# Performance work log

Hardware: AMD Instinct MI355X
Metric: run time of the kernel (lower is better)

Reference implementation:

```python
import jax, jax.numpy as jnp
import numpy as np

V, E, H, L, P, N = 500000, 128, 128, 10, 10, 50
SCALE = 1e-4


def setup_inputs() -> dict:
    key = jax.random.key(0)
    ks = jax.random.split(key, 10)
    initrange = 0.5 / E
    return {
        "phr_inds": jax.random.randint(ks[0], (L,), 0, V),
        "pos_inds": jax.random.randint(ks[1], (P, L), 0, V),
        "neg_inds": jax.random.randint(ks[2], (N, L), 0, V),
        "u_emb": jax.random.uniform(ks[3], (V, E), minval=-initrange, maxval=initrange, dtype=jnp.float32),
        "v_emb": jax.random.uniform(ks[4], (V, E), minval=-initrange, maxval=initrange, dtype=jnp.float32),
        "w_ih": jax.random.uniform(ks[5], (3 * H, E), minval=-SCALE, maxval=SCALE, dtype=jnp.float32),
        "w_hh": jax.random.uniform(ks[6], (3 * H, H), minval=-SCALE, maxval=SCALE, dtype=jnp.float32),
        "b_ih": jax.random.uniform(ks[7], (3 * H,), minval=-SCALE, maxval=SCALE, dtype=jnp.float32),
        "b_hh": jax.random.uniform(ks[8], (3 * H,), minval=-SCALE, maxval=SCALE, dtype=jnp.float32),
        "h0": jax.random.uniform(ks[9], (H,), minval=-SCALE, maxval=SCALE, dtype=jnp.float32),
    }


def _gru_last_hidden(x, h0, w_ih, w_hh, b_ih, b_hh):
    # x: [B, L, E] -> last hidden state [B, H]; torch GRU gate order (r, z, n)
    B = x.shape[0]
    gi = jnp.einsum('ble,ge->blg', x, w_ih) + b_ih  # input projections precomputed [B, L, 3H]
    h = jnp.broadcast_to(h0, (B, h0.shape[-1]))

    def step(h, gi_t):
        gh = h @ w_hh.T + b_hh
        ir, iz, in_ = jnp.split(gi_t, 3, axis=-1)
        hr, hz, hn = jnp.split(gh, 3, axis=-1)
        r = jax.nn.sigmoid(ir + hr)
        z = jax.nn.sigmoid(iz + hz)
        n = jnp.tanh(in_ + r * hn)
        return (1.0 - z) * n + z * h, None

    h, _ = jax.lax.scan(step, h, jnp.swapaxes(gi, 0, 1))  # scan over time
    return h


def reference(phr_inds, pos_inds, neg_inds, u_emb, v_emb, w_ih, w_hh, b_ih, b_hh, h0):
    rnn_size = h0.shape[-1]
    phr_x = u_emb[phr_inds][None]   # [1, L, E] (center phrase uses u table)
    pos_x = v_emb[pos_inds]         # [P, L, E]
    neg_x = v_emb[neg_inds]         # [N, L, E]
    x = jnp.concatenate([phr_x, pos_x, neg_x], axis=0)  # batch all GRU calls together
    enc = _gru_last_hidden(x, h0, w_ih, w_hh, b_ih, b_hh)
    node = enc[0]
    n_pos = pos_inds.shape[0]
    pos_e, neg_e = enc[1:1 + n_pos], enc[1 + n_pos:]
    # dot_product_sum(exp=False): sum_i <node, pos_i> / rnn_size
    pos_loss = ((node * pos_e).sum(-1) / rnn_size).sum()
    # dot_product_sum(exp=True): exp(s) masked to s>0, then summed
    s = (node * neg_e).sum(-1) / rnn_size
    neg_sum = (jnp.exp(s) * (s > 0.0).astype(s.dtype)).sum()
    neg_loss = -jnp.log(1.0 + neg_sum)
    return -(neg_loss + pos_loss)
```

## Files before the change

kernel.cpp:

```cpp
#include <hip/hip_runtime.h>
#include <hip/hip_bf16.h>
#include <math.h>

#define V_SZ 500000
#define E_SZ 128
#define H_SZ 128
#define L_SZ 10
#define P_SZ 10
#define N_SZ 50
#define NSEQ (P_SZ + N_SZ)
#define NBLK 60
#define TPB  384

#define SIG_STRIDE 8
#define FLAG_MAGIC 0x9E370000u

#define GI_STR 388
#define XS_STR 136

typedef __attribute__((ext_vector_type(8))) short bf16x8;
typedef __attribute__((ext_vector_type(4))) float f32x4;

#define MFMA(a, b, c) __builtin_amdgcn_mfma_f32_16x16x32_bf16((a), (b), (c), 0, 0, 0)

__device__ __forceinline__ float sigmoidf(float x) {
    return 1.0f / (1.0f + expf(-x));
}

__device__ __forceinline__ unsigned short f2bf(float f) {
    __hip_bfloat16 h = __float2bfloat16(f);
    unsigned short u;
    __builtin_memcpy(&u, &h, sizeof(u));
    return u;
}

__device__ __forceinline__ unsigned f2bf2(float lo, float hi) {
    float2 v = make_float2(lo, hi);
    __hip_bfloat162 h2 = __float22bfloat162_rn(v);
    unsigned u;
    __builtin_memcpy(&u, &h2, sizeof(u));
    return u;
}

__device__ __forceinline__ uint2 f2bf4(float4 v) {
    uint2 r;
    r.x = f2bf2(v.x, v.y);
    r.y = f2bf2(v.z, v.w);
    return r;
}

__global__ __launch_bounds__(TPB) void gru_fused(
    const int*   __restrict__ phr_inds,
    const int*   __restrict__ pos_inds,
    const int*   __restrict__ neg_inds,
    const float* __restrict__ u_emb,
    const float* __restrict__ v_emb,
    const float* __restrict__ w_ih,
    const float* __restrict__ w_hh,
    const float* __restrict__ b_ih,
    const float* __restrict__ b_hh,
    const float* __restrict__ h0,
    unsigned long long* __restrict__ sig,
    float*       __restrict__ out)
{
    __shared__ __align__(16) unsigned short stage_u[384 * E_SZ];
    __shared__ __align__(16) unsigned short xs_bf16[2][16 * XS_STR];
    __shared__ __align__(16) float          gh_s[2][3 * H_SZ];
    __shared__ __align__(16) unsigned short hs_bf16[2][H_SZ];
    __shared__ __align__(16) float          node[2][H_SZ];

    float* gi_all = (float*)stage_u;

    const int bj   = blockIdx.x;
    const int seqB = bj + 1;
    const int t    = threadIdx.x;
    const int lane = t & 63;
    const int wv   = t >> 6;
    const int kg   = lane >> 4;
    const int col  = lane & 15;
    const int arow = wv * 64 + col;

    for (int i = t; i < 2 * L_SZ * 32; i += TPB) {
        const int r  = i >> 5;
        const int e4 = i & 31;
        const int g  = (r < L_SZ) ? 0 : 1;
        const int l  = (r < L_SZ) ? r : r - L_SZ;
        int idx; const float* emb;
        if (g == 0)             { idx = phr_inds[l];                       emb = u_emb; }
        else if (seqB <= P_SZ)  { idx = pos_inds[(seqB - 1) * L_SZ + l];   emb = v_emb; }
        else                    { idx = neg_inds[(seqB - 1 - P_SZ) * L_SZ + l]; emb = v_emb; }
        const float4 v = *reinterpret_cast<const float4*>(emb + (size_t)idx * E_SZ + e4 * 4);
        *reinterpret_cast<uint2*>((char*)&xs_bf16[g][0] + l * (XS_STR * 2) + e4 * 8) = f2bf4(v);
    }

    const int gseq = t >> 7;
    const int gu   = t & 127;
    float bih_r = 0.f, bih_z = 0.f, bih_n = 0.f;
    float bhh_r = 0.f, bhh_z = 0.f, bhh_n = 0.f;
    float h_reg = 0.f;
    if (t < 2 * H_SZ) {
        bih_r = b_ih[gu]; bih_z = b_ih[gu + 128]; bih_n = b_ih[gu + 256];
        bhh_r = b_hh[gu]; bhh_z = b_hh[gu + 128]; bhh_n = b_hh[gu + 256];
        h_reg = h0[gu];
        hs_bf16[gseq][gu] = f2bf(h_reg);
    }

    bf16x8 aih[4][4], ahh[4][4];
    #pragma unroll
    for (int m = 0; m < 2; ++m) {
        const float* W = (m == 0) ? w_ih : w_hh;
        #pragma unroll 8
        for (int q = 0; q < (384 * E_SZ / 4) / TPB; ++q) {
            const int fi = q * TPB + t;
            const int lr = fi >> 5;
            const int e4 = fi & 31;
            const float4 v = *reinterpret_cast<const float4*>(W + (size_t)lr * E_SZ + e4 * 4);
            const int byte = (lr * 256 + e4 * 8) ^ ((lr & 7) << 4);
            *reinterpret_cast<uint2*>((char*)stage_u + byte) = f2bf4(v);
        }
        __syncthreads();

        #pragma unroll
        for (int mb = 0; mb < 4; ++mb) {
            const int lr = arow + mb * 16;
            #pragma unroll
            for (int kb = 0; kb < 4; ++kb) {
                const int byte = (lr * 256 + kb * 64 + kg * 16) ^ ((lr & 7) << 4);
                const bf16x8 f = *reinterpret_cast<const bf16x8*>((const char*)stage_u + byte);
                if (m == 0) aih[mb][kb] = f;
                else        ahh[mb][kb] = f;
            }
        }
        __syncthreads();
    }

    #pragma unroll
    for (int g = 0; g < 2; ++g) {
        f32x4 g0 = {0.f,0.f,0.f,0.f}, g1 = {0.f,0.f,0.f,0.f};
        f32x4 g2 = {0.f,0.f,0.f,0.f}, g3 = {0.f,0.f,0.f,0.f};
        #pragma unroll
        for (int kb = 0; kb < 4; ++kb) {
            const bf16x8 xb = *reinterpret_cast<const bf16x8*>(
                (const char*)&xs_bf16[g][0] + col * (XS_STR * 2) + kb * 64 + kg * 16);
            g0 = MFMA(aih[0][kb], xb, g0);
            g1 = MFMA(aih[1][kb], xb, g1);
            g2 = MFMA(aih[2][kb], xb, g2);
            g3 = MFMA(aih[3][kb], xb, g3);
        }
        const int rb = wv * 64 + kg * 4;
        *reinterpret_cast<f32x4*>(&gi_all[g * (16 * GI_STR) + col * GI_STR + rb     ]) = g0;
        *reinterpret_cast<f32x4*>(&gi_all[g * (16 * GI_STR) + col * GI_STR + rb + 16]) = g1;
        *reinterpret_cast<f32x4*>(&gi_all[g * (16 * GI_STR) + col * GI_STR + rb + 32]) = g2;
        *reinterpret_cast<f32x4*>(&gi_all[g * (16 * GI_STR) + col * GI_STR + rb + 48]) = g3;
    }

    for (int l = 0; l < L_SZ; ++l) {
        f32x4 a0 = {0.f,0.f,0.f,0.f}, a1 = {0.f,0.f,0.f,0.f};
        f32x4 a2 = {0.f,0.f,0.f,0.f}, a3 = {0.f,0.f,0.f,0.f};
        #pragma unroll
        for (int kb = 0; kb < 4; ++kb) {
            const bf16x8 bh = *reinterpret_cast<const bf16x8*>(
                (const char*)&hs_bf16[col & 1][0] + kb * 64 + kg * 16);
            a0 = MFMA(ahh[0][kb], bh, a0);
            a1 = MFMA(ahh[1][kb], bh, a1);
            a2 = MFMA(ahh[2][kb], bh, a2);
            a3 = MFMA(ahh[3][kb], bh, a3);
        }
        if (col < 2) {
            const int rb = wv * 64 + kg * 4;
            *reinterpret_cast<f32x4*>(&gh_s[col][rb     ]) = a0;
            *reinterpret_cast<f32x4*>(&gh_s[col][rb + 16]) = a1;
            *reinterpret_cast<f32x4*>(&gh_s[col][rb + 32]) = a2;
            *reinterpret_cast<f32x4*>(&gh_s[col][rb + 48]) = a3;
        }
        __syncthreads();

        if (t < 2 * H_SZ) {
            const float* gi = &gi_all[gseq * (16 * GI_STR) + l * GI_STR];
            const float* gh = &gh_s[gseq][0];
            const float r = sigmoidf(gi[gu      ] + bih_r + (gh[gu      ] + bhh_r));
            const float z = sigmoidf(gi[gu + 128] + bih_z + (gh[gu + 128] + bhh_z));
            const float n = tanhf  (gi[gu + 256] + bih_n + r * (gh[gu + 256] + bhh_n));
            h_reg = (1.0f - z) * n + z * h_reg;
            if (l < L_SZ - 1) hs_bf16[gseq][gu] = f2bf(h_reg);
            else              node[gseq][gu]   = h_reg;
        }
        __syncthreads();
    }

    if (t >= 64) return;

    float d = node[0][t] * node[1][t] + node[0][t + 64] * node[1][t + 64];
    #pragma unroll
    for (int off = 32; off > 0; off >>= 1) d += __shfl_down(d, off);
    const float s_own = d * (1.0f / (float)H_SZ);

    if (bj != 0) {
        if (t == 0) {
            const unsigned long long v =
                ((unsigned long long)(FLAG_MAGIC + (unsigned)bj) << 32) |
                (unsigned long long)__float_as_uint(s_own);
            atomicExch(&sig[bj * SIG_STRIDE], v);
        }
        return;
    }

    float sv = 0.0f;
    if (t == 0) sv = s_own;
    else if (t < NSEQ) {
        const unsigned want = FLAG_MAGIC + (unsigned)t;
        unsigned long long v;
        do {
            v = atomicAdd(&sig[t * SIG_STRIDE], 0ull);
            if ((unsigned)(v >> 32) == want) break;
            __builtin_amdgcn_s_sleep(2);
        } while (true);
        sv = __uint_as_float((unsigned)(v & 0xFFFFFFFFull));
    }

    float vp = 0.0f, vn = 0.0f;
    if (t < P_SZ)      vp = sv;
    else if (t < NSEQ) vn = (sv > 0.0f) ? expf(sv) : 0.0f;

    #pragma unroll
    for (int off = 32; off > 0; off >>= 1) {
        vp += __shfl_down(vp, off);
        vn += __shfl_down(vn, off);
    }
    if (t == 0) {
        out[0] = logf(1.0f + vn) - vp;
    }
}

extern "C" void kernel_launch(void* const* d_in, const int* in_sizes, int n_in,
                              void* d_out, int out_size, void* d_ws, size_t ws_size,
                              hipStream_t stream) {
    const int*   phr_inds = (const int*)  d_in[0];
    const int*   pos_inds = (const int*)  d_in[1];
    const int*   neg_inds = (const int*)  d_in[2];
    const float* u_emb    = (const float*)d_in[3];
    const float* v_emb    = (const float*)d_in[4];
    const float* w_ih     = (const float*)d_in[5];
    const float* w_hh     = (const float*)d_in[6];
    const float* b_ih     = (const float*)d_in[7];
    const float* b_hh     = (const float*)d_in[8];
    const float* h0       = (const float*)d_in[9];

    unsigned long long* sig = (unsigned long long*)d_ws;

    gru_fused<<<NBLK, TPB, 0, stream>>>(phr_inds, pos_inds, neg_inds,
                                        u_emb, v_emb, w_ih, w_hh, b_ih, b_hh, h0,
                                        sig, (float*)d_out);
}
```

Baseline: 20.48 us.

## Overlap w_hh staging loads with input-projection MFMAs using separate gi buffer

Moves the input-projection results into a dedicated shared buffer so the staging area can be reused for w_hh while the gi MFMAs run. The w_hh global loads are split into four chunks and software-pipelined with two register buffers, interleaved with the gi MFMA halves, to hide global-load latency behind compute. This raises LDS usage and register pressure (16 float4 load buffers live alongside the A fragments), which may reduce occupancy or cause spills.

Result: no change. 20.49 us (+0.0%).

```diff
diff --git a/kernel.cpp b/kernel.cpp
--- a/kernel.cpp
+++ b/kernel.cpp
@@ -64,12 +64,11 @@
     float*       __restrict__ out)
 {
     __shared__ __align__(16) unsigned short stage_u[384 * E_SZ];
+    __shared__ __align__(16) float          gi_all[2 * L_SZ * GI_STR];
     __shared__ __align__(16) unsigned short xs_bf16[2][16 * XS_STR];
     __shared__ __align__(16) float          gh_s[2][3 * H_SZ];
     __shared__ __align__(16) unsigned short hs_bf16[2][H_SZ];
     __shared__ __align__(16) float          node[2][H_SZ];
-
-    float* gi_all = (float*)stage_u;
 
     const int bj   = blockIdx.x;
     const int seqB = bj + 1;
@@ -106,52 +105,94 @@
     }
 
     bf16x8 aih[4][4], ahh[4][4];
-    #pragma unroll
-    for (int m = 0; m < 2; ++m) {
-        const float* W = (m == 0) ? w_ih : w_hh;
-        #pragma unroll 8
-        for (int q = 0; q < (384 * E_SZ / 4) / TPB; ++q) {
-            const int fi = q * TPB + t;
-            const int lr = fi >> 5;
-            const int e4 = fi & 31;
-            const float4 v = *reinterpret_cast<const float4*>(W + (size_t)lr * E_SZ + e4 * 4);
-            const int byte = (lr * 256 + e4 * 8) ^ ((lr & 7) << 4);
-            *reinterpret_cast<uint2*>((char*)stage_u + byte) = f2bf4(v);
-        }
-        __syncthreads();
-
-        #pragma unroll
-        for (int mb = 0; mb < 4; ++mb) {
-            const int lr = arow + mb * 16;
-            #pragma unroll
-            for (int kb = 0; kb < 4; ++kb) {
-                const int byte = (lr * 256 + kb * 64 + kg * 16) ^ ((lr & 7) << 4);
-                const bf16x8 f = *reinterpret_cast<const bf16x8*>((const char*)stage_u + byte);
-                if (m == 0) aih[mb][kb] = f;
-                else        ahh[mb][kb] = f;
-            }
-        }
-        __syncthreads();
-    }
-
-    #pragma unroll
-    for (int g = 0; g < 2; ++g) {
-        f32x4 g0 = {0.f,0.f,0.f,0.f}, g1 = {0.f,0.f,0.f,0.f};
-        f32x4 g2 = {0.f,0.f,0.f,0.f}, g3 = {0.f,0.f,0.f,0.f};
+    #pragma unroll 8
+    for (int q = 0; q < (384 * E_SZ / 4) / TPB; ++q) {
+        const int fi = q * TPB + t;
+        const int lr = fi >> 5;
+        const int e4 = fi & 31;
+        const float4 v = *reinterpret_cast<const float4*>(w_ih + (size_t)lr * E_SZ + e4 * 4);
+        const int byte = (lr * 256 + e4 * 8) ^ ((lr & 7) << 4);
+        *reinterpret_cast<uint2*>((char*)stage_u + byte) = f2bf4(v);
+    }
+    __syncthreads();
+
+    #pragma unroll
+    for (int mb = 0; mb < 4; ++mb) {
+        const int lr = arow + mb * 16;
         #pragma unroll
         for (int kb = 0; kb < 4; ++kb) {
-            const bf16x8 xb = *reinterpret_cast<const bf16x8*>(
-                (const char*)&xs_bf16[g][0] + col * (XS_STR * 2) + kb * 64 + kg * 16);
-            g0 = MFMA(aih[0][kb], xb, g0);
-            g1 = MFMA(aih[1][kb], xb, g1);
-            g2 = MFMA(aih[2][kb], xb, g2);
-            g3 = MFMA(aih[3][kb], xb, g3);
-        }
-        const int rb = wv * 64 + kg * 4;
-        *reinterpret_cast<f32x4*>(&gi_all[g * (16 * GI_STR) + col * GI_STR + rb     ]) = g0;
-        *reinterpret_cast<f32x4*>(&gi_all[g * (16 * GI_STR) + col * GI_STR + rb + 16]) = g1;
-        *reinterpret_cast<f32x4*>(&gi_all[g * (16 * GI_STR) + col * GI_STR + rb + 32]) = g2;
-        *reinterpret_cast<f32x4*>(&gi_all[g * (16 * GI_STR) + col * GI_STR + rb + 48]) = g3;
+            const int byte = (lr * 256 + kb * 64 + kg * 16) ^ ((lr & 7) << 4);
+            aih[mb][kb] = *reinterpret_cast<const bf16x8*>((const char*)stage_u + byte);
+        }
+    }
+    __syncthreads();
+
+#define LOADW(buf, c)                                                          \
+    _Pragma("unroll")                                                          \
+    for (int q = 0; q < 8; ++q) {                                              \
+        const int fi = ((c) * 8 + q) * TPB + t;                                \
+        (buf)[q] = *reinterpret_cast<const float4*>(                           \
+            w_hh + (size_t)(fi >> 5) * E_SZ + (fi & 31) * 4);                  \
+    }
+#define WRITEW(buf, c)                                                         \
+    _Pragma("unroll")                                                          \
+    for (int q = 0; q < 8; ++q) {                                              \
+        const int fi = ((c) * 8 + q) * TPB + t;                                \
+        const int lr = fi >> 5;                                                \
+        const int byte = (lr * 256 + (fi & 31) * 8) ^ ((lr & 7) << 4);         \
+        *reinterpret_cast<uint2*>((char*)stage_u + byte) = f2bf4((buf)[q]);    \
+    }
+#define GI_HALF(g, h)                                                          \
+    _Pragma("unroll")                                                          \
+    for (int kbi = 0; kbi < 2; ++kbi) {                                        \
+        const int kb = (h) * 2 + kbi;                                          \
+        const bf16x8 xb = *reinterpret_cast<const bf16x8*>(                    \
+            (const char*)&xs_bf16[(g)][0] + col * (XS_STR * 2) + kb * 64 + kg * 16); \
+        ac0 = MFMA(aih[0][kb], xb, ac0);                                       \
+        ac1 = MFMA(aih[1][kb], xb, ac1);                                       \
+        ac2 = MFMA(aih[2][kb], xb, ac2);                                       \
+        ac3 = MFMA(aih[3][kb], xb, ac3);                                       \
+    }
+#define GI_WRITE(g)                                                            \
+    if (col < L_SZ) {                                                          \
+        const int rb   = wv * 64 + kg * 4;                                     \
+        float* gp = &gi_all[(g) * (L_SZ * GI_STR) + col * GI_STR];             \
+        *reinterpret_cast<f32x4*>(gp + rb     ) = ac0;                         \
+        *reinterpret_cast<f32x4*>(gp + rb + 16) = ac1;                         \
+        *reinterpret_cast<f32x4*>(gp + rb + 32) = ac2;                         \
+        *reinterpret_cast<f32x4*>(gp + rb + 48) = ac3;                         \
+    }
+
+    {
+        float4 va[8], vb[8];
+        f32x4 ac0, ac1, ac2, ac3;
+        LOADW(va, 0);
+        LOADW(vb, 1);
+        ac0 = ac1 = ac2 = ac3 = (f32x4){0.f, 0.f, 0.f, 0.f};
+        GI_HALF(0, 0);
+        WRITEW(va, 0);
+        LOADW(va, 2);
+        GI_HALF(0, 1);
+        GI_WRITE(0);
+        WRITEW(vb, 1);
+        LOADW(vb, 3);
+        ac0 = ac1 = ac2 = ac3 = (f32x4){0.f, 0.f, 0.f, 0.f};
+        GI_HALF(1, 0);
+        WRITEW(va, 2);
+        GI_HALF(1, 1);
+        GI_WRITE(1);
+        WRITEW(vb, 3);
+    }
+    __syncthreads();
+
+    #pragma unroll
+    for (int mb = 0; mb < 4; ++mb) {
+        const int lr = arow + mb * 16;
+        #pragma unroll
+        for (int kb = 0; kb < 4; ++kb) {
+            const int byte = (lr * 256 + kb * 64 + kg * 16) ^ ((lr & 7) << 4);
+            ahh[mb][kb] = *reinterpret_cast<const bf16x8*>((const char*)stage_u + byte);
+        }
     }
 
     for (int l = 0; l < L_SZ; ++l) {
@@ -176,7 +217,7 @@
         __syncthreads();
 
         if (t < 2 * H_SZ) {
-            const float* gi = &gi_all[gseq * (16 * GI_STR) + l * GI_STR];
+            const float* gi = &gi_all[gseq * (L_SZ * GI_STR) + l * GI_STR];
             const float* gh = &gh_s[gseq][0];
             const float r = sigmoidf(gi[gu      ] + bih_r + (gh[gu      ] + bhh_r));
             const float z = sigmoidf(gi[gu + 128] + bih_z + (gh[gu + 128] + bhh_z));
```
